# Kernel tuning notes

Hardware: AMD Instinct MI355X
Metric: run time of the kernel (lower is better)

Reference implementation:

```python
import jax, jax.numpy as jnp
import numpy as np

V, C, T, H, L, B = 32000, 1024, 1024, 16, 4, 4
HD = C // H
FF = 4 * C
LN_EPS = 1e-5


def _sinusoidal(block_size, n_embd):
    pos = np.arange(block_size, dtype=np.float32)[:, None]
    div = np.exp(np.arange(0, n_embd, 2, dtype=np.float32) * (-np.log(10000.0) / n_embd))
    enc = np.zeros((block_size, n_embd), dtype=np.float32)
    enc[:, 0::2] = np.sin(pos * div)
    enc[:, 1::2] = np.cos(pos * div)
    return jnp.asarray(enc)


def setup_inputs() -> dict:
    key = jax.random.key(0)
    ks = jax.random.split(key, 12)
    std = 0.02
    n = lambda k, s: jax.random.normal(k, s, jnp.float32) * std
    return {
        'idx': jax.random.randint(ks[0], (B, T), 0, V),
        'emb': n(ks[1], (V, C)),
        'pos_enc': _sinusoidal(T, C),
        'Wq': n(ks[2], (L, C, C)),
        'Wk': n(ks[3], (L, C, C)),
        'Wv': n(ks[4], (L, C, C)),
        'Wo': n(ks[5], (L, C, C)),
        'bo': jnp.zeros((L, C), jnp.float32),
        'W1': n(ks[6], (L, C, FF)),
        'b1': jnp.zeros((L, FF), jnp.float32),
        'W2': n(ks[7], (L, FF, C)),
        'b2': jnp.zeros((L, C), jnp.float32),
        'ln1_g': jnp.ones((L, C), jnp.float32),
        'ln1_b': jnp.zeros((L, C), jnp.float32),
        'ln2_g': jnp.ones((L, C), jnp.float32),
        'ln2_b': jnp.zeros((L, C), jnp.float32),
        'lnf_g': jnp.ones((C,), jnp.float32),
        'lnf_b': jnp.zeros((C,), jnp.float32),
        'Wlm': n(ks[8], (C, V)),
        'blm': jnp.zeros((V,), jnp.float32),
    }


def _layer_norm(x, g, b):
    m = jnp.mean(x, -1, keepdims=True)
    v = jnp.var(x, -1, keepdims=True)
    return (x - m) * jax.lax.rsqrt(v + LN_EPS) * g + b


def _forward(idx, emb, pos_enc, Wq, Wk, Wv, Wo, bo, W1, b1, W2, b2,
             ln1_g, ln1_b, ln2_g, ln2_b, lnf_g, lnf_b, Wlm, blm):
    Bv, Tv = idx.shape
    x = emb[idx] + pos_enc[None, :Tv, :]  # [B,T,C]
    mask = jnp.tril(jnp.ones((Tv, Tv), dtype=bool))
    scale = HD ** -0.5

    def block(x, p):
        wq, wk, wv, wo, bov, w1, b1v, w2, b2v, g1, bn1, g2, bn2 = p
        h = _layer_norm(x, g1, bn1)
        q = jnp.einsum('btc,chd->bhtd', h, wq.reshape(C, H, HD))
        k = jnp.einsum('btc,chd->bhtd', h, wk.reshape(C, H, HD))
        v = jnp.einsum('btc,chd->bhtd', h, wv.reshape(C, H, HD))
        wei = jnp.einsum('bhqd,bhkd->bhqk', q, k) * scale
        wei = jnp.where(mask, wei, -jnp.inf)
        wei = jax.nn.softmax(wei, axis=-1)
        o = jnp.einsum('bhqk,bhkd->bhqd', wei, v)
        o = o.transpose(0, 2, 1, 3).reshape(Bv, Tv, C)
        x = x + o @ wo + bov
        h2 = _layer_norm(x, g2, bn2)
        x = x + jax.nn.gelu(h2 @ w1 + b1v, approximate=False) @ w2 + b2v
        return x, None

    x, _ = jax.lax.scan(block, x, (Wq, Wk, Wv, Wo, bo, W1, b1, W2, b2,
                                   ln1_g, ln1_b, ln2_g, ln2_b))
    x = _layer_norm(x, lnf_g, lnf_b)
    return x @ Wlm + blm  # [B,T,V]


def reference(idx, emb, pos_enc, Wq, Wk, Wv, Wo, bo, W1, b1, W2, b2,
              ln1_g, ln1_b, ln2_g, ln2_b, lnf_g, lnf_b, Wlm, blm):
    return _forward(idx, emb, pos_enc, Wq, Wk, Wv, Wo, bo, W1, b1, W2, b2,
                    ln1_g, ln1_b, ln2_g, ln2_b, lnf_g, lnf_b, Wlm, blm)
```

## Files before the change

kernel.cpp:

```cpp
#include <hip/hip_runtime.h>

#define V_  32000
#define C_  1024
#define T_  1024
#define H_  16
#define L_  4
#define B_  4
#define HD_ 64
#define FF_ 4096
#define M_  (B_ * T_)

typedef __attribute__((ext_vector_type(8))) short bf16x8;
typedef __attribute__((ext_vector_type(4))) float f32x4;
typedef unsigned short u16;

#define FENCE() asm volatile("" ::: "memory")
#define BAR()  do { FENCE(); __builtin_amdgcn_s_barrier(); FENCE(); } while (0)
#define VMW(n) asm volatile("s_waitcnt vmcnt(" #n ")" ::: "memory")

__device__ __forceinline__ u16 f2bf(float f) {
  unsigned u = __builtin_bit_cast(unsigned, f);
  u += 0x7fffu + ((u >> 16) & 1u);
  return (u16)(u >> 16);
}

__device__ __forceinline__ void gload16(const u16* g, u16* l) {
  __builtin_amdgcn_global_load_lds(
      (const __attribute__((address_space(1))) void*)g,
      (__attribute__((address_space(3))) void*)l, 16, 0, 0);
}

__global__ __launch_bounds__(256)
void embed_kernel(const int* __restrict__ idx, const float* __restrict__ emb,
                  const float* __restrict__ pos, float* __restrict__ x) {
  int row = blockIdx.x;
  int t = row & (T_ - 1);
  int tok = idx[row];
  float4 e = reinterpret_cast<const float4*>(emb + (size_t)tok * C_)[threadIdx.x];
  float4 p = reinterpret_cast<const float4*>(pos + (size_t)t * C_)[threadIdx.x];
  float4 r;
  r.x = e.x + p.x; r.y = e.y + p.y; r.z = e.z + p.z; r.w = e.w + p.w;
  reinterpret_cast<float4*>(x + (size_t)row * C_)[threadIdx.x] = r;
}

__global__ __launch_bounds__(256)
void ln_kernel(const float* __restrict__ xin, const float* __restrict__ g,
               const float* __restrict__ bta, u16* __restrict__ out) {
  const int w = threadIdx.x >> 6, lane = threadIdx.x & 63;
  const int row = blockIdx.x * 4 + w;
  const float4* xr = reinterpret_cast<const float4*>(xin + (size_t)row * C_);
  float4 xv[4];
  float s = 0.f, ss = 0.f;
  #pragma unroll
  for (int j = 0; j < 4; ++j) {
    xv[j] = xr[lane + 64 * j];
    s  += xv[j].x + xv[j].y + xv[j].z + xv[j].w;
    ss += xv[j].x * xv[j].x + xv[j].y * xv[j].y + xv[j].z * xv[j].z + xv[j].w * xv[j].w;
  }
  #pragma unroll
  for (int d = 1; d < 64; d <<= 1) {
    s  += __shfl_xor(s, d, 64);
    ss += __shfl_xor(ss, d, 64);
  }
  float mean = s * (1.0f / C_);
  float var  = ss * (1.0f / C_) - mean * mean;
  float rstd = rsqrtf(var + 1e-5f);
  #pragma unroll
  for (int j = 0; j < 4; ++j) {
    float4 gv = reinterpret_cast<const float4*>(g)[lane + 64 * j];
    float4 bv = reinterpret_cast<const float4*>(bta)[lane + 64 * j];
    union { u16 u[4]; uint2 v; } pk;
    pk.u[0] = f2bf((xv[j].x - mean) * rstd * gv.x + bv.x);
    pk.u[1] = f2bf((xv[j].y - mean) * rstd * gv.y + bv.y);
    pk.u[2] = f2bf((xv[j].z - mean) * rstd * gv.z + bv.z);
    pk.u[3] = f2bf((xv[j].w - mean) * rstd * gv.w + bv.w);
    *reinterpret_cast<uint2*>(&out[(size_t)row * C_ + (lane + 64 * j) * 4]) = pk.v;
  }
}

__global__ __launch_bounds__(256)
void wtrans_kernel(const float* __restrict__ W, u16* __restrict__ Wt, int K, int N,
                   size_t dstBS) {
  const float* src = W + (size_t)blockIdx.z * K * N;
  u16* dst = Wt + (size_t)blockIdx.z * dstBS;
  __shared__ float tile[32][33];
  int k0 = blockIdx.y * 32, n0 = blockIdx.x * 32;
  int tx = threadIdx.x & 31, ty = threadIdx.x >> 5;
  #pragma unroll
  for (int i = 0; i < 4; ++i)
    tile[ty * 4 + i][tx] = src[(size_t)(k0 + ty * 4 + i) * N + n0 + tx];
  __syncthreads();
  int n = threadIdx.x >> 3, q = threadIdx.x & 7;
  union { u16 u[4]; uint2 v; } pk;
  #pragma unroll
  for (int j = 0; j < 4; ++j) pk.u[j] = f2bf(tile[4 * q + j][n]);
  *reinterpret_cast<uint2*>(&dst[(size_t)(n0 + n) * K + k0 + 4 * q]) = pk.v;
}

template <int MODE, int GROUP_M>
__global__ __launch_bounds__(256)
void gemm_bt(const u16* __restrict__ A, const u16* __restrict__ Bt,
             const float* __restrict__ bias, const float* __restrict__ resid,
             void* __restrict__ Cout, u16* __restrict__ vtb,
             int M, int N, int K) {
  __shared__ u16 As[128 * 32];
  __shared__ u16 Bs[128 * 32];
  const int nbm = M >> 7, nbn = N >> 7;
  const int nwg = nbm * nbn;
  const int bid = blockIdx.x;
  const int chunk = nwg >> 3;
  const int swz = (bid & 7) * chunk + (bid >> 3);
  const int gsz = GROUP_M * nbn;
  const int grp = swz / gsz, rem = swz % gsz;
  const int by = grp * GROUP_M + (rem % GROUP_M);
  const int bx = rem / GROUP_M;
  const int m0 = by * 128, n0 = bx * 128;

  const int tid = threadIdx.x, lane = tid & 63, w = tid >> 6;
  const int wr = w >> 1, wc = w & 1;
  const int frow = lane & 15, fk = (lane >> 4) * 8;
  const int srow = lane >> 2, scol = (lane & 3) * 8;

  f32x4 acc[4][4];
  #pragma unroll
  for (int i = 0; i < 4; ++i)
    #pragma unroll
    for (int j = 0; j < 4; ++j) acc[i][j] = (f32x4)0.0f;

  for (int k0 = 0; k0 < K; k0 += 32) {
    gload16(&A [(size_t)(m0 + w * 32 +      srow) * K + k0 + scol], As + w * 1024);
    gload16(&A [(size_t)(m0 + w * 32 + 16 + srow) * K + k0 + scol], As + w * 1024 + 512);
    gload16(&Bt[(size_t)(n0 + w * 32 +      srow) * K + k0 + scol], Bs + w * 1024);
    gload16(&Bt[(size_t)(n0 + w * 32 + 16 + srow) * K + k0 + scol], Bs + w * 1024 + 512);
    __syncthreads();

    bf16x8 af[4], bfr[4];
    #pragma unroll
    for (int mi = 0; mi < 4; ++mi)
      af[mi] = *reinterpret_cast<const bf16x8*>(&As[(wr * 64 + mi * 16 + frow) * 32 + fk]);
    #pragma unroll
    for (int ni = 0; ni < 4; ++ni)
      bfr[ni] = *reinterpret_cast<const bf16x8*>(&Bs[(wc * 64 + ni * 16 + frow) * 32 + fk]);
    #pragma unroll
    for (int mi = 0; mi < 4; ++mi)
      #pragma unroll
      for (int ni = 0; ni < 4; ++ni)
        acc[mi][ni] = __builtin_amdgcn_mfma_f32_16x16x32_bf16(af[mi], bfr[ni], acc[mi][ni], 0, 0, 0);
    __syncthreads();
  }

  u16* outb = (u16*)Cout;
  float* outf = (float*)Cout;
  const bool vblk = (MODE == 4) && (n0 >= 2 * C_);
  #pragma unroll
  for (int mi = 0; mi < 4; ++mi) {
    #pragma unroll
    for (int ni = 0; ni < 4; ++ni) {
      int orow = m0 + wr * 64 + mi * 16 + ((lane >> 4) << 2);
      int ocol = n0 + wc * 64 + ni * 16 + (lane & 15);
      float bv = 0.0f;
      if constexpr (MODE == 1 || MODE == 2 || MODE == 3) bv = bias[ocol];
      if constexpr (MODE == 4) {
        if (vblk) {
          int vcol = ocol - 2 * C_;
          int hh = vcol >> 6, d = vcol & 63;
          int bb = orow >> 10, t0 = orow & (T_ - 1);
          union { u16 u[4]; uint2 v2; } pk;
          #pragma unroll
          for (int r = 0; r < 4; ++r) pk.u[r] = f2bf(acc[mi][ni][r]);
          *reinterpret_cast<uint2*>(
              &vtb[(((size_t)bb * H_ + hh) * HD_ + d) * T_ + t0]) = pk.v2;
        } else {
          #pragma unroll
          for (int r = 0; r < 4; ++r)
            outb[(size_t)(orow + r) * (2 * C_) + ocol] = f2bf(acc[mi][ni][r]);
        }
      } else {
        #pragma unroll
        for (int r = 0; r < 4; ++r) {
          size_t off = (size_t)(orow + r) * N + ocol;
          float val = acc[mi][ni][r] + bv;
          if constexpr (MODE == 0) {
            outb[off] = f2bf(val);
          } else if constexpr (MODE == 1) {
            outf[off] = val + resid[off];
          } else if constexpr (MODE == 2) {
            val = 0.5f * val * (1.0f + erff(val * 0.70710678118654752f));
            outb[off] = f2bf(val);
          } else if constexpr (MODE == 3) {
            outf[off] = val;
          }
        }
      }
    }
  }
}

template <int MODE>
__global__ __launch_bounds__(512, 2)
void gemm8(const u16* __restrict__ A, const u16* __restrict__ Bt,
           const float* __restrict__ bias, const float* __restrict__ resid,
           void* __restrict__ Cout, int M, int N, int K) {
  __shared__ u16 lds8[65536];
  const int nbm = M >> 8, nbn = N >> 8;
  const int nwg = nbm * nbn;
  const int chunk = nwg >> 3;
  const int bid = blockIdx.x;
  const int swz = (bid & 7) * chunk + (bid >> 3);
  const int gsz = 4 * nbn;
  const int grp = swz / gsz, rem = swz % gsz;
  const int by = grp * 4 + (rem & 3);
  const int bx = rem >> 2;
  const int m0 = by << 8, n0 = bx << 8;

  const int tid = threadIdx.x, lane = tid & 63, w = tid >> 6;
  const int wm = w >> 2, wn = w & 3;
  const int fr = lane & 15, kgb = (lane >> 4) * 16;
  const int scolz = 8 * ((lane & 7) ^ (lane >> 3));
  const int NT = K >> 6;
  const int NI = NT >> 1;

  f32x4 acc[8][4];
  #pragma unroll
  for (int i = 0; i < 8; ++i)
    #pragma unroll
    for (int j = 0; j < 4; ++j) acc[i][j] = (f32x4)0.0f;

  auto ldr = [&](int d, int isB, int row, int cb) -> bf16x8 {
    int bo = row * 128 + (cb ^ ((row & 7) << 4));
    const char* base = (const char*)lds8 + d * 65536 + isB * 32768 +
                       (isB ? (wn >> 1) : wm) * 16384;
    return *reinterpret_cast<const bf16x8*>(base + bo);
  };
  auto stage_half = [&](const u16* grow0, u16* ldst) {
    #pragma unroll
    for (int p = 0; p < 2; ++p) {
      int r = (p * 8 + w) * 8 + (lane >> 3);
      gload16(grow0 + (size_t)r * K + scolz, ldst + (p * 8 + w) * 512);
    }
  };
  auto stageA = [&](int d, int h, int t) {
    stage_half(&A[(size_t)(m0 + h * 128) * K + t * 64],
               lds8 + d * 32768 + h * 8192);
  };
  auto stageB = [&](int d, int h, int t) {
    stage_half(&Bt[(size_t)(n0 + h * 128) * K + t * 64],
               lds8 + d * 32768 + 16384 + h * 8192);
  };

  bf16x8 af[2][2], bfr[4][2];

#define LDA_Q(d, q) do {                                   \
    af[0][0] = ldr(d, 0, (q) * 32 + fr,      kgb);         \
    af[0][1] = ldr(d, 0, (q) * 32 + fr,      64 + kgb);    \
    af[1][0] = ldr(d, 0, (q) * 32 + 16 + fr, kgb);         \
    af[1][1] = ldr(d, 0, (q) * 32 + 16 + fr, 64 + kgb);    \
  } while (0)
#define LDB_ALL(d) do {                                    \
    _Pragma("unroll")                                      \
    for (int nj = 0; nj < 4; ++nj) {                       \
      bfr[nj][0] = ldr(d, 1, (wn & 1) * 64 + nj * 16 + fr, kgb);      \
      bfr[nj][1] = ldr(d, 1, (wn & 1) * 64 + nj * 16 + fr, 64 + kgb); \
    }                                                      \
  } while (0)
#define MFMA_Q(q) do {                                     \
    __builtin_amdgcn_s_setprio(1);                         \
    _Pragma("unroll")                                      \
    for (int lmi = 0; lmi < 2; ++lmi)                      \
      _Pragma("unroll")                                    \
      for (int nj = 0; nj < 4; ++nj)                       \
        _Pragma("unroll")                                  \
        for (int ks = 0; ks < 2; ++ks)                     \
          acc[2 * (q) + lmi][nj] = __builtin_amdgcn_mfma_f32_16x16x32_bf16( \
              af[lmi][ks], bfr[nj][ks], acc[2 * (q) + lmi][nj], 0, 0, 0);   \
    __builtin_amdgcn_s_setprio(0);                         \
  } while (0)

  stageB(0, 0, 0); stageB(0, 1, 0);
  stageA(0, 0, 0); stageA(0, 1, 0);
  stageB(1, 0, 1); stageB(1, 1, 1);
  VMW(4);
  BAR();

  for (int i = 0; i < NI; ++i) {
    const int a = 2 * i, b = 2 * i + 1;
    const bool pa = (a + 2 < NT), pb = (b + 2 < NT);
    LDB_ALL(0); LDA_Q(0, 0);
    stageA(1, 0, b);
    BAR(); MFMA_Q(0); BAR();
    LDA_Q(0, 1);
    stageA(1, 1, b);
    if (pa) stageB(0, 0, a + 2);
    BAR(); MFMA_Q(1); BAR();
    LDA_Q(0, 2);
    if (pa) stageB(0, 1, a + 2);
    BAR(); MFMA_Q(2); BAR();
    LDA_Q(0, 3);
    BAR(); MFMA_Q(3);
    if (pa) { VMW(4); } else { VMW(0); }
    BAR();
    LDB_ALL(1); LDA_Q(1, 0);
    if (pa) stageA(0, 0, a + 2);
    BAR(); MFMA_Q(0); BAR();
    LDA_Q(1, 1);
    if (pa) stageA(0, 1, a + 2);
    BAR(); MFMA_Q(1); BAR();
    LDA_Q(1, 2);
    if (pb) stageB(1, 0, b + 2);
    BAR(); MFMA_Q(2); BAR();
    LDA_Q(1, 3);
    if (pb) stageB(1, 1, b + 2);
    BAR(); MFMA_Q(3);
    if (pb) { VMW(4); } else { VMW(0); }
    BAR();
  }
#undef LDA_Q
#undef LDB_ALL
#undef MFMA_Q

  u16* outb = (u16*)Cout;
  float* outf = (float*)Cout;
  #pragma unroll
  for (int mi = 0; mi < 8; ++mi) {
    #pragma unroll
    for (int nj = 0; nj < 4; ++nj) {
      int orow = m0 + wm * 128 + mi * 16 + ((lane >> 4) << 2);
      int ocol = n0 + wn * 64 + nj * 16 + (lane & 15);
      float bv = 0.0f;
      if constexpr (MODE != 0) bv = bias[ocol];
      #pragma unroll
      for (int r = 0; r < 4; ++r) {
        size_t off = (size_t)(orow + r) * N + ocol;
        float val = acc[mi][nj][r] + bv;
        if constexpr (MODE == 0) {
          outb[off] = f2bf(val);
        } else if constexpr (MODE == 1) {
          outf[off] = val + resid[off];
        } else if constexpr (MODE == 2) {
          val = 0.5f * val * (1.0f + erff(val * 0.70710678118654752f));
          outb[off] = f2bf(val);
        } else {
          outf[off] = val;
        }
      }
    }
  }
}

template <int MODE>
__global__ __launch_bounds__(256)
void gemm_legacy(const u16* __restrict__ A, const float* __restrict__ Bw,
                 const float* __restrict__ bias, const float* __restrict__ resid,
                 void* __restrict__ Cout, int M, int N, int K) {
  __shared__ u16 As[128][40];
  __shared__ u16 Bs[128][40];
  const int m0 = blockIdx.y * 128, n0 = blockIdx.x * 128;
  const int tid = threadIdx.x, lane = tid & 63, w = tid >> 6;
  const int wr = w >> 1, wc = w & 1;
  const int row = lane & 15, kk8 = (lane >> 4) * 8;
  f32x4 acc[4][4];
  #pragma unroll
  for (int i = 0; i < 4; ++i)
    #pragma unroll
    for (int j = 0; j < 4; ++j) acc[i][j] = (f32x4)0.0f;
  for (int k0 = 0; k0 < K; k0 += 32) {
    #pragma unroll
    for (int i = 0; i < 2; ++i) {
      int e = (tid + i * 256) * 8;
      int r = e >> 5, c = e & 31;
      *reinterpret_cast<uint4*>(&As[r][c]) =
        *reinterpret_cast<const uint4*>(&A[(size_t)(m0 + r) * K + k0 + c]);
    }
    #pragma unroll
    for (int i = 0; i < 4; ++i) {
      int e = (tid + i * 256) * 4;
      int kr = e >> 7, c = e & 127;
      float4 bv = *reinterpret_cast<const float4*>(&Bw[(size_t)(k0 + kr) * N + n0 + c]);
      Bs[c + 0][kr] = f2bf(bv.x);
      Bs[c + 1][kr] = f2bf(bv.y);
      Bs[c + 2][kr] = f2bf(bv.z);
      Bs[c + 3][kr] = f2bf(bv.w);
    }
    __syncthreads();
    bf16x8 af[4], bfr[4];
    #pragma unroll
    for (int mi = 0; mi < 4; ++mi)
      af[mi] = *reinterpret_cast<const bf16x8*>(&As[wr * 64 + mi * 16 + row][kk8]);
    #pragma unroll
    for (int ni = 0; ni < 4; ++ni)
      bfr[ni] = *reinterpret_cast<const bf16x8*>(&Bs[wc * 64 + ni * 16 + row][kk8]);
    #pragma unroll
    for (int mi = 0; mi < 4; ++mi)
      #pragma unroll
      for (int ni = 0; ni < 4; ++ni)
        acc[mi][ni] = __builtin_amdgcn_mfma_f32_16x16x32_bf16(af[mi], bfr[ni], acc[mi][ni], 0, 0, 0);
    __syncthreads();
  }
  u16* outb = (u16*)Cout;
  float* outf = (float*)Cout;
  #pragma unroll
  for (int mi = 0; mi < 4; ++mi) {
    #pragma unroll
    for (int ni = 0; ni < 4; ++ni) {
      int orow = m0 + wr * 64 + mi * 16 + ((lane >> 4) << 2);
      int ocol = n0 + wc * 64 + ni * 16 + (lane & 15);
      float bv = 0.0f;
      if constexpr (MODE != 0) bv = bias[ocol];
      #pragma unroll
      for (int r = 0; r < 4; ++r) {
        size_t off = (size_t)(orow + r) * N + ocol;
        float val = acc[mi][ni][r] + bv;
        if constexpr (MODE == 0) outb[off] = f2bf(val);
        else if constexpr (MODE == 1) outf[off] = val + resid[off];
        else if constexpr (MODE == 2) {
          val = 0.5f * val * (1.0f + erff(val * 0.70710678118654752f));
          outb[off] = f2bf(val);
        } else outf[off] = val;
      }
    }
  }
}

__global__ __launch_bounds__(512)
void attn_kernel(const u16* __restrict__ qg, const u16* __restrict__ kg,
                 const u16* __restrict__ vt, u16* __restrict__ og) {
  const int bh = blockIdx.y;
  const int q0 = blockIdx.x * 128;
  const int b = bh >> 4;
  const int tid = threadIdx.x, lane = tid & 63, w = tid >> 6;
  const int fr = lane & 15, kk8 = (lane >> 4) * 8;
  __shared__ u16 KS[2][4096];
  __shared__ u16 VS[2][4096];
  __shared__ u16 Ps[8][16][72];

  const int ldq = 2 * C_;
  const size_t baseq = ((size_t)b * T_) * ldq + (bh & 15) * HD_;
  const u16* qbase = qg + baseq;
  const u16* kbase = kg + baseq;
  const u16* vbase = vt + ((size_t)bh * HD_) * T_;
  const size_t baseo = ((size_t)b * T_) * C_ + (bh & 15) * HD_;
  const int qw = q0 + w * 16;

  bf16x8 qf[2];
  #pragma unroll
  for (int s = 0; s < 2; ++s)
    qf[s] = *reinterpret_cast<const bf16x8*>(&qbase[(size_t)(qw + fr) * ldq + s * 32 + kk8]);

  const int srow8 = lane >> 3;
  const int scol = 8 * ((lane & 7) ^ srow8);
  auto stageKV = [&](int d, int kv0) {
    int rr = w * 8 + srow8;
    gload16(kbase + (size_t)(kv0 + rr) * ldq + scol, &KS[d][w * 512]);
    gload16(vbase + (size_t)rr * T_ + kv0 + scol,    &VS[d][w * 512]);
  };
  auto ldS = [&](const u16* base, int row, int cu) -> bf16x8 {
    return *reinterpret_cast<const bf16x8*>(&base[row * 64 + (cu ^ ((row & 7) << 3))]);
  };

  f32x4 acc_o[4];
  #pragma unroll
  for (int dt = 0; dt < 4; ++dt) acc_o[dt] = (f32x4)0.0f;
  float m_run[4] = {-1e30f, -1e30f, -1e30f, -1e30f};
  float l_run[4] = {0.f, 0.f, 0.f, 0.f};
  const float scale = 0.125f;

  const int kv_end = q0 + 128;
  stageKV(0, 0);
  VMW(0); BAR();

  int cur = 0;
  for (int kv0 = 0; kv0 < kv_end; kv0 += 64, cur ^= 1) {
    if (kv0 + 64 < kv_end) stageKV(cur ^ 1, kv0 + 64);

    f32x4 sacc[4];
    #pragma unroll
    for (int nt = 0; nt < 4; ++nt) sacc[nt] = (f32x4)0.0f;
    #pragma unroll
    for (int nt = 0; nt < 4; ++nt)
      #pragma unroll
      for (int s = 0; s < 2; ++s) {
        bf16x8 kf = ldS(KS[cur], nt * 16 + fr, s * 32 + kk8);
        sacc[nt] = __builtin_amdgcn_mfma_f32_16x16x32_bf16(qf[s], kf, sacc[nt], 0, 0, 0);
      }

    #pragma unroll
    for (int i = 0; i < 4; ++i) {
      int qrow = qw + ((lane >> 4) << 2) + i;
      float sv[4], pv[4];
      #pragma unroll
      for (int nt = 0; nt < 4; ++nt) {
        sv[nt] = sacc[nt][i] * scale;
        if (kv0 + nt * 16 + (lane & 15) > qrow) sv[nt] = -1e30f;
      }
      float mx = fmaxf(fmaxf(sv[0], sv[1]), fmaxf(sv[2], sv[3]));
      #pragma unroll
      for (int d = 1; d < 16; d <<= 1) mx = fmaxf(mx, __shfl_xor(mx, d, 64));
      float mnew = fmaxf(m_run[i], mx);
      float rsum = 0.0f;
      #pragma unroll
      for (int nt = 0; nt < 4; ++nt) { pv[nt] = __expf(sv[nt] - mnew); rsum += pv[nt]; }
      float alpha = __expf(m_run[i] - mnew);
      #pragma unroll
      for (int d = 1; d < 16; d <<= 1) rsum += __shfl_xor(rsum, d, 64);
      l_run[i] = l_run[i] * alpha + rsum;
      m_run[i] = mnew;
      #pragma unroll
      for (int dt = 0; dt < 4; ++dt) acc_o[dt][i] *= alpha;
      #pragma unroll
      for (int nt = 0; nt < 4; ++nt)
        Ps[w][((lane >> 4) << 2) + i][(lane & 15) + nt * 16] = f2bf(pv[nt]);
    }

    #pragma unroll
    for (int dt = 0; dt < 4; ++dt)
      #pragma unroll
      for (int s = 0; s < 2; ++s) {
        bf16x8 pf = *reinterpret_cast<const bf16x8*>(&Ps[w][fr][s * 32 + kk8]);
        bf16x8 vf = ldS(VS[cur], dt * 16 + fr, s * 32 + kk8);
        acc_o[dt] = __builtin_amdgcn_mfma_f32_16x16x32_bf16(pf, vf, acc_o[dt], 0, 0, 0);
      }
    VMW(0); BAR();
  }

  #pragma unroll
  for (int dt = 0; dt < 4; ++dt)
    #pragma unroll
    for (int i = 0; i < 4; ++i) {
      int r = qw + ((lane >> 4) << 2) + i;
      float val = acc_o[dt][i] / l_run[i];
      og[baseo + (size_t)r * C_ + dt * 16 + (lane & 15)] = f2bf(val);
    }
}

__global__ __launch_bounds__(256)
void attn_legacy(const u16* __restrict__ qg, const u16* __restrict__ kg,
                 const u16* __restrict__ vg, u16* __restrict__ og, int ldq) {
  const int bh = blockIdx.y;
  const int b = bh >> 4, hh = bh & 15;
  const int q0 = blockIdx.x * 64;
  const int tid = threadIdx.x, lane = tid & 63, w = tid >> 6;
  const int row = lane & 15, kk8 = (lane >> 4) * 8;
  __shared__ u16 Ks[64][72];
  __shared__ u16 Vt[64][72];
  __shared__ u16 Ps[4][16][72];

  const size_t basei = ((size_t)b * T_) * ldq + hh * HD_;
  const size_t baseo = ((size_t)b * T_) * C_ + hh * HD_;
  const int qw = q0 + w * 16;

  bf16x8 qf[2];
  #pragma unroll
  for (int s = 0; s < 2; ++s)
    qf[s] = *reinterpret_cast<const bf16x8*>(&qg[basei + (size_t)(qw + row) * ldq + s * 32 + kk8]);

  f32x4 acc_o[4];
  #pragma unroll
  for (int dt = 0; dt < 4; ++dt) acc_o[dt] = (f32x4)0.0f;
  float m_run[4] = {-1e30f, -1e30f, -1e30f, -1e30f};
  float l_run[4] = {0.f, 0.f, 0.f, 0.f};
  const float scale = 0.125f;

  const int sc = (tid & 7) * 8;
  const int kv_end = q0 + 64;
  for (int kv0 = 0; kv0 < kv_end; kv0 += 64) {
    #pragma unroll
    for (int p = 0; p < 2; ++p) {
      int sr = p * 32 + (tid >> 3);
      *reinterpret_cast<uint4*>(&Ks[sr][sc]) =
        *reinterpret_cast<const uint4*>(&kg[basei + (size_t)(kv0 + sr) * ldq + sc]);
      union { uint4 u4; u16 us[8]; } vv;
      vv.u4 = *reinterpret_cast<const uint4*>(&vg[basei + (size_t)(kv0 + sr) * ldq + sc]);
      #pragma unroll
      for (int j = 0; j < 8; ++j) Vt[sc + j][sr] = vv.us[j];
    }
    __syncthreads();

    f32x4 sacc[4];
    #pragma unroll
    for (int nt = 0; nt < 4; ++nt) sacc[nt] = (f32x4)0.0f;
    #pragma unroll
    for (int nt = 0; nt < 4; ++nt)
      #pragma unroll
      for (int s = 0; s < 2; ++s) {
        bf16x8 kf = *reinterpret_cast<const bf16x8*>(&Ks[nt * 16 + row][s * 32 + kk8]);
        sacc[nt] = __builtin_amdgcn_mfma_f32_16x16x32_bf16(qf[s], kf, sacc[nt], 0, 0, 0);
      }

    #pragma unroll
    for (int i = 0; i < 4; ++i) {
      int qrow = qw + ((lane >> 4) << 2) + i;
      float sv[4], pv[4];
      #pragma unroll
      for (int nt = 0; nt < 4; ++nt) {
        sv[nt] = sacc[nt][i] * scale;
        if (kv0 + nt * 16 + (lane & 15) > qrow) sv[nt] = -1e30f;
      }
      float mx = fmaxf(fmaxf(sv[0], sv[1]), fmaxf(sv[2], sv[3]));
      #pragma unroll
      for (int d = 1; d < 16; d <<= 1) mx = fmaxf(mx, __shfl_xor(mx, d, 64));
      float mnew = fmaxf(m_run[i], mx);
      float rsum = 0.0f;
      #pragma unroll
      for (int nt = 0; nt < 4; ++nt) { pv[nt] = __expf(sv[nt] - mnew); rsum += pv[nt]; }
      float alpha = __expf(m_run[i] - mnew);
      #pragma unroll
      for (int d = 1; d < 16; d <<= 1) rsum += __shfl_xor(rsum, d, 64);
      l_run[i] = l_run[i] * alpha + rsum;
      m_run[i] = mnew;
      #pragma unroll
      for (int dt = 0; dt < 4; ++dt) acc_o[dt][i] *= alpha;
      #pragma unroll
      for (int nt = 0; nt < 4; ++nt)
        Ps[w][((lane >> 4) << 2) + i][(lane & 15) + nt * 16] = f2bf(pv[nt]);
    }

    #pragma unroll
    for (int dt = 0; dt < 4; ++dt)
      #pragma unroll
      for (int s = 0; s < 2; ++s) {
        bf16x8 pf = *reinterpret_cast<const bf16x8*>(&Ps[w][row][s * 32 + kk8]);
        bf16x8 vf = *reinterpret_cast<const bf16x8*>(&Vt[dt * 16 + row][s * 32 + kk8]);
        acc_o[dt] = __builtin_amdgcn_mfma_f32_16x16x32_bf16(pf, vf, acc_o[dt], 0, 0, 0);
      }
    __syncthreads();
  }

  #pragma unroll
  for (int dt = 0; dt < 4; ++dt)
    #pragma unroll
    for (int i = 0; i < 4; ++i) {
      int r = qw + ((lane >> 4) << 2) + i;
      float val = acc_o[dt][i] / l_run[i];
      og[baseo + (size_t)r * C_ + dt * 16 + (lane & 15)] = f2bf(val);
    }
}

extern "C" void kernel_launch(void* const* d_in, const int* in_sizes, int n_in,
                              void* d_out, int out_size, void* d_ws, size_t ws_size,
                              hipStream_t stream) {
  const int*   idx  = (const int*)d_in[0];
  const float* emb  = (const float*)d_in[1];
  const float* pos  = (const float*)d_in[2];
  const float* Wq   = (const float*)d_in[3];
  const float* Wk   = (const float*)d_in[4];
  const float* Wv   = (const float*)d_in[5];
  const float* Wo   = (const float*)d_in[6];
  const float* bo   = (const float*)d_in[7];
  const float* W1   = (const float*)d_in[8];
  const float* b1   = (const float*)d_in[9];
  const float* W2   = (const float*)d_in[10];
  const float* b2   = (const float*)d_in[11];
  const float* ln1g = (const float*)d_in[12];
  const float* ln1b = (const float*)d_in[13];
  const float* ln2g = (const float*)d_in[14];
  const float* ln2b = (const float*)d_in[15];
  const float* lnfg = (const float*)d_in[16];
  const float* lnfb = (const float*)d_in[17];
  const float* Wlm  = (const float*)d_in[18];
  const float* blm  = (const float*)d_in[19];

  char* ws = (char*)d_ws;
  float* x    = (float*)ws;
  u16*   h    = (u16*)(ws + (16u << 20));
  u16*   qkv  = (u16*)(ws + (24u << 20));
  u16*   vtb  = (u16*)(ws + (40u << 20));
  u16*   ob   = (u16*)(ws + (48u << 20));
  u16*   ffb  = (u16*)(ws + (24u << 20));

  u16* WqkvT = (u16*)(ws + (56u  << 20));
  u16* WoT   = (u16*)(ws + (80u  << 20));
  u16* W1T   = (u16*)(ws + (88u  << 20));
  u16* W2T   = (u16*)(ws + (120u << 20));
  u16* WlmT  = (u16*)(ws + (152u << 20));
  const size_t WS_NEED = (152ull << 20) + 2ull * C_ * V_;

  dim3 blk(256), blk8(512), blkA(512);
  const int nQKV = (M_ / 128) * (3 * C_ / 128);
  const int nCC  = (M_ / 128) * (C_ / 128);
  const int nF1_8 = (M_ / 256) * (FF_ / 256);
  const int nLM_8 = (M_ / 256) * (V_ / 256);
  dim3 gA(T_ / 128, B_ * H_);

  embed_kernel<<<M_, blk, 0, stream>>>(idx, emb, pos, x);

  if (ws_size >= WS_NEED) {
    const size_t s3 = (size_t)3 * C_ * C_;
    wtrans_kernel<<<dim3(C_ / 32,  C_ / 32, L_), blk, 0, stream>>>(Wq, WqkvT,              C_, C_, s3);
    wtrans_kernel<<<dim3(C_ / 32,  C_ / 32, L_), blk, 0, stream>>>(Wk, WqkvT + (size_t)C_ * C_,     C_, C_, s3);
    wtrans_kernel<<<dim3(C_ / 32,  C_ / 32, L_), blk, 0, stream>>>(Wv, WqkvT + (size_t)2 * C_ * C_, C_, C_, s3);
    wtrans_kernel<<<dim3(C_ / 32,  C_ / 32, L_), blk, 0, stream>>>(Wo, WoT, C_, C_, (size_t)C_ * C_);
    wtrans_kernel<<<dim3(FF_ / 32, C_ / 32, L_), blk, 0, stream>>>(W1, W1T, C_, FF_, (size_t)C_ * FF_);
    wtrans_kernel<<<dim3(C_ / 32, FF_ / 32, L_), blk, 0, stream>>>(W2, W2T, FF_, C_, (size_t)C_ * FF_);
    wtrans_kernel<<<dim3(V_ / 32,  C_ / 32, 1),  blk, 0, stream>>>(Wlm, WlmT, C_, V_, (size_t)C_ * V_);

    for (int l = 0; l < L_; ++l) {
      ln_kernel<<<M_ / 4, blk, 0, stream>>>(x, ln1g + l * C_, ln1b + l * C_, h);
      gemm_bt<4, 8><<<nQKV, blk, 0, stream>>>(h, WqkvT + (size_t)l * s3, nullptr, nullptr, qkv, vtb, M_, 3 * C_, C_);
      attn_kernel<<<gA, blkA, 0, stream>>>(qkv, qkv + C_, vtb, ob);
      gemm_bt<1, 8><<<nCC, blk, 0, stream>>>(ob, WoT + (size_t)l * C_ * C_, bo + l * C_, x, x, nullptr, M_, C_, C_);
      ln_kernel<<<M_ / 4, blk, 0, stream>>>(x, ln2g + l * C_, ln2b + l * C_, h);
      gemm8<2><<<nF1_8, blk8, 0, stream>>>(h, W1T + (size_t)l * C_ * FF_, b1 + l * FF_, nullptr, ffb, M_, FF_, C_);
      gemm_bt<1, 8><<<nCC, blk, 0, stream>>>(ffb, W2T + (size_t)l * C_ * FF_, b2 + l * C_, x, x, nullptr, M_, C_, FF_);
    }
    ln_kernel<<<M_ / 4, blk, 0, stream>>>(x, lnfg, lnfb, h);
    gemm8<3><<<nLM_8, blk8, 0, stream>>>(h, WlmT, blm, nullptr, (float*)d_out, M_, V_, C_);
  } else {
    float* xr = x;
    u16* qb = qkv;
    u16* kb = qkv + (size_t)M_ * C_;
    u16* vb = (u16*)(ws + (40u << 20));
    dim3 gC(C_ / 128, M_ / 128);
    dim3 gF(FF_ / 128, M_ / 128);
    dim3 gV(V_ / 128, M_ / 128);
    dim3 gAl(T_ / 64, B_ * H_);
    for (int l = 0; l < L_; ++l) {
      ln_kernel<<<M_ / 4, blk, 0, stream>>>(xr, ln1g + l * C_, ln1b + l * C_, h);
      gemm_legacy<0><<<gC, blk, 0, stream>>>(h, Wq + (size_t)l * C_ * C_, nullptr, nullptr, qb, M_, C_, C_);
      gemm_legacy<0><<<gC, blk, 0, stream>>>(h, Wk + (size_t)l * C_ * C_, nullptr, nullptr, kb, M_, C_, C_);
      gemm_legacy<0><<<gC, blk, 0, stream>>>(h, Wv + (size_t)l * C_ * C_, nullptr, nullptr, vb, M_, C_, C_);
      attn_legacy<<<gAl, blk, 0, stream>>>(qb, kb, vb, ob, C_);
      gemm_legacy<1><<<gC, blk, 0, stream>>>(ob, Wo + (size_t)l * C_ * C_, bo + l * C_, xr, xr, M_, C_, C_);
      ln_kernel<<<M_ / 4, blk, 0, stream>>>(xr, ln2g + l * C_, ln2b + l * C_, h);
      gemm_legacy<2><<<gF, blk, 0, stream>>>(h, W1 + (size_t)l * C_ * FF_, b1 + l * FF_, nullptr, ffb, M_, FF_, C_);
      gemm_legacy<1><<<gC, blk, 0, stream>>>(ffb, W2 + (size_t)l * FF_ * C_, b2 + l * C_, xr, xr, M_, C_, FF_);
    }
    ln_kernel<<<M_ / 4, blk, 0, stream>>>(xr, lnfg, lnfb, h);
    gemm_legacy<3><<<gV, blk, 0, stream>>>(h, Wlm, blm, nullptr, (float*)d_out, M_, V_, C_);
  }
}
```

Measured before the change: 1.609 ms.

## Double-buffer LDS tiles in gemm_bt and fuse first LayerNorm into embedding

The gemm_bt main loop now uses two LDS buffers. It issues the global-to-LDS loads for the next K tile before computing on the current one, so memory latency can overlap the MFMA work, and it needs one barrier per iteration instead of two. This doubles LDS use per block, which could lower occupancy. Separately, the embedding kernel optionally computes the layer-0 LayerNorm in place, which removes one ln_kernel launch and a re-read of x.

Measured after the change: 1.541 ms. -4.3%, faster.

```diff
diff --git a/kernel.cpp b/kernel.cpp
--- a/kernel.cpp
+++ b/kernel.cpp
@@ -30,9 +30,12 @@
       (__attribute__((address_space(3))) void*)l, 16, 0, 0);
 }
 
+template <int FUSE_LN>
 __global__ __launch_bounds__(256)
 void embed_kernel(const int* __restrict__ idx, const float* __restrict__ emb,
-                  const float* __restrict__ pos, float* __restrict__ x) {
+                  const float* __restrict__ pos, float* __restrict__ x,
+                  const float* __restrict__ g, const float* __restrict__ bta,
+                  u16* __restrict__ hout) {
   int row = blockIdx.x;
   int t = row & (T_ - 1);
   int tok = idx[row];
@@ -41,6 +44,33 @@
   float4 r;
   r.x = e.x + p.x; r.y = e.y + p.y; r.z = e.z + p.z; r.w = e.w + p.w;
   reinterpret_cast<float4*>(x + (size_t)row * C_)[threadIdx.x] = r;
+  if constexpr (FUSE_LN) {
+    int tid = threadIdx.x;
+    float s  = r.x + r.y + r.z + r.w;
+    float ss = r.x * r.x + r.y * r.y + r.z * r.z + r.w * r.w;
+    #pragma unroll
+    for (int d = 1; d < 64; d <<= 1) {
+      s  += __shfl_xor(s, d, 64);
+      ss += __shfl_xor(ss, d, 64);
+    }
+    __shared__ float rs[4], rss[4];
+    int w = tid >> 6, lane = tid & 63;
+    if (lane == 0) { rs[w] = s; rss[w] = ss; }
+    __syncthreads();
+    s  = rs[0] + rs[1] + rs[2] + rs[3];
+    ss = rss[0] + rss[1] + rss[2] + rss[3];
+    float mean = s * (1.0f / C_);
+    float var  = ss * (1.0f / C_) - mean * mean;
+    float rstd = rsqrtf(var + 1e-5f);
+    float4 gv = reinterpret_cast<const float4*>(g)[tid];
+    float4 bv = reinterpret_cast<const float4*>(bta)[tid];
+    union { u16 u[4]; uint2 v; } pk;
+    pk.u[0] = f2bf((r.x - mean) * rstd * gv.x + bv.x);
+    pk.u[1] = f2bf((r.y - mean) * rstd * gv.y + bv.y);
+    pk.u[2] = f2bf((r.z - mean) * rstd * gv.z + bv.z);
+    pk.u[3] = f2bf((r.w - mean) * rstd * gv.w + bv.w);
+    *reinterpret_cast<uint2*>(&hout[(size_t)row * C_ + tid * 4]) = pk.v;
+  }
 }
 
 __global__ __launch_bounds__(256)
@@ -103,8 +133,8 @@
              const float* __restrict__ bias, const float* __restrict__ resid,
              void* __restrict__ Cout, u16* __restrict__ vtb,
              int M, int N, int K) {
-  __shared__ u16 As[128 * 32];
-  __shared__ u16 Bs[128 * 32];
+  __shared__ u16 As[2][128 * 32];
+  __shared__ u16 Bs[2][128 * 32];
   const int nbm = M >> 7, nbn = N >> 7;
   const int nwg = nbm * nbn;
   const int bid = blockIdx.x;
@@ -127,26 +157,35 @@
     #pragma unroll
     for (int j = 0; j < 4; ++j) acc[i][j] = (f32x4)0.0f;
 
-  for (int k0 = 0; k0 < K; k0 += 32) {
-    gload16(&A [(size_t)(m0 + w * 32 +      srow) * K + k0 + scol], As + w * 1024);
-    gload16(&A [(size_t)(m0 + w * 32 + 16 + srow) * K + k0 + scol], As + w * 1024 + 512);
-    gload16(&Bt[(size_t)(n0 + w * 32 +      srow) * K + k0 + scol], Bs + w * 1024);
-    gload16(&Bt[(size_t)(n0 + w * 32 + 16 + srow) * K + k0 + scol], Bs + w * 1024 + 512);
-    __syncthreads();
+  auto stage = [&](int d, int k0) {
+    gload16(&A [(size_t)(m0 + w * 32 +      srow) * K + k0 + scol], As[d] + w * 1024);
+    gload16(&A [(size_t)(m0 + w * 32 + 16 + srow) * K + k0 + scol], As[d] + w * 1024 + 512);
+    gload16(&Bt[(size_t)(n0 + w * 32 +      srow) * K + k0 + scol], Bs[d] + w * 1024);
+    gload16(&Bt[(size_t)(n0 + w * 32 + 16 + srow) * K + k0 + scol], Bs[d] + w * 1024 + 512);
+  };
+
+  const int NT = K >> 5;
+  stage(0, 0);
+  VMW(0); BAR();
+
+  for (int kt = 0; kt < NT; ++kt) {
+    const int cur = kt & 1;
+    if (kt + 1 < NT) stage(cur ^ 1, (kt + 1) << 5);
 
     bf16x8 af[4], bfr[4];
     #pragma unroll
     for (int mi = 0; mi < 4; ++mi)
-      af[mi] = *reinterpret_cast<const bf16x8*>(&As[(wr * 64 + mi * 16 + frow) * 32 + fk]);
+      af[mi] = *reinterpret_cast<const bf16x8*>(&As[cur][(wr * 64 + mi * 16 + frow) * 32 + fk]);
     #pragma unroll
     for (int ni = 0; ni < 4; ++ni)
-      bfr[ni] = *reinterpret_cast<const bf16x8*>(&Bs[(wc * 64 + ni * 16 + frow) * 32 + fk]);
+      bfr[ni] = *reinterpret_cast<const bf16x8*>(&Bs[cur][(wc * 64 + ni * 16 + frow) * 32 + fk]);
     #pragma unroll
     for (int mi = 0; mi < 4; ++mi)
       #pragma unroll
       for (int ni = 0; ni < 4; ++ni)
         acc[mi][ni] = __builtin_amdgcn_mfma_f32_16x16x32_bf16(af[mi], bfr[ni], acc[mi][ni], 0, 0, 0);
-    __syncthreads();
+
+    VMW(0); BAR();
   }
 
   u16* outb = (u16*)Cout;
@@ -681,10 +720,9 @@
   const int nLM_8 = (M_ / 256) * (V_ / 256);
   dim3 gA(T_ / 128, B_ * H_);
 
-  embed_kernel<<<M_, blk, 0, stream>>>(idx, emb, pos, x);
-
   if (ws_size >= WS_NEED) {
     const size_t s3 = (size_t)3 * C_ * C_;
+    embed_kernel<1><<<M_, blk, 0, stream>>>(idx, emb, pos, x, ln1g, ln1b, h);
     wtrans_kernel<<<dim3(C_ / 32,  C_ / 32, L_), blk, 0, stream>>>(Wq, WqkvT,              C_, C_, s3);
     wtrans_kernel<<<dim3(C_ / 32,  C_ / 32, L_), blk, 0, stream>>>(Wk, WqkvT + (size_t)C_ * C_,     C_, C_, s3);
     wtrans_kernel<<<dim3(C_ / 32,  C_ / 32, L_), blk, 0, stream>>>(Wv, WqkvT + (size_t)2 * C_ * C_, C_, C_, s3);
@@ -694,7 +732,8 @@
     wtrans_kernel<<<dim3(V_ / 32,  C_ / 32, 1),  blk, 0, stream>>>(Wlm, WlmT, C_, V_, (size_t)C_ * V_);
 
     for (int l = 0; l < L_; ++l) {
-      ln_kernel<<<M_ / 4, blk, 0, stream>>>(x, ln1g + l * C_, ln1b + l * C_, h);
+      if (l > 0)
+        ln_kernel<<<M_ / 4, blk, 0, stream>>>(x, ln1g + l * C_, ln1b + l * C_, h);
       gemm_bt<4, 8><<<nQKV, blk, 0, stream>>>(h, WqkvT + (size_t)l * s3, nullptr, nullptr, qkv, vtb, M_, 3 * C_, C_);
       attn_kernel<<<gA, blkA, 0, stream>>>(qkv, qkv + C_, vtb, ob);
       gemm_bt<1, 8><<<nCC, blk, 0, stream>>>(ob, WoT + (size_t)l * C_ * C_, bo + l * C_, x, x, nullptr, M_, C_, C_);
@@ -705,6 +744,7 @@
     ln_kernel<<<M_ / 4, blk, 0, stream>>>(x, lnfg, lnfb, h);
     gemm8<3><<<nLM_8, blk8, 0, stream>>>(h, WlmT, blm, nullptr, (float*)d_out, M_, V_, C_);
   } else {
+    embed_kernel<0><<<M_, blk, 0, stream>>>(idx, emb, pos, x, nullptr, nullptr, nullptr);
     float* xr = x;
     u16* qb = qkv;
     u16* kb = qkv + (size_t)M_ * C_;
```
